# Kernel tuning notes

Measured on AMD Instinct MI355X. Metric: run time of the kernel, lower is better.

The kernel has to match this reference:

```python
import jax, jax.numpy as jnp
import numpy as np

B, L, D, H = 8, 1024, 1024, 16
DPH = D // H  # 64


def setup_inputs() -> dict:
    key = jax.random.key(0)
    ks = jax.random.split(key, 12)
    s = 1.0 / np.sqrt(D)
    return {
        "key": jax.random.normal(ks[0], (B, L, D), jnp.float32),
        "value": jax.random.normal(ks[1], (B, L, D), jnp.float32),
        "query": jax.random.normal(ks[2], (B, L, D), jnp.float32),
        "attn_mask": jax.random.randint(ks[3], (B, L, L), 0, 2) > 0,
        "Wq": jax.random.normal(ks[4], (D, D), jnp.float32) * s,
        "bq": jnp.zeros((D,), jnp.float32),
        "Wk": jax.random.normal(ks[5], (D, D), jnp.float32) * s,
        "bk": jnp.zeros((D,), jnp.float32),
        "Wv": jax.random.normal(ks[6], (D, D), jnp.float32) * s,
        "bv": jnp.zeros((D,), jnp.float32),
        "Wo": jax.random.normal(ks[7], (D, D), jnp.float32) * s,
        "bo": jnp.zeros((D,), jnp.float32),
        "gamma": jnp.ones((D,), jnp.float32),
        "beta": jnp.zeros((D,), jnp.float32),
    }


def _layer_norm(x, gamma, beta, eps=1e-5):
    mu = jnp.mean(x, axis=-1, keepdims=True)
    var = jnp.var(x, axis=-1, keepdims=True)
    return (x - mu) * jax.lax.rsqrt(var + eps) * gamma + beta


def reference(key, value, query, attn_mask, Wq, bq, Wk, bk, Wv, bv, Wo, bo, gamma, beta):
    residual = query
    k = key @ Wk + bk      # [B, L, D]
    v = value @ Wv + bv
    q = query @ Wq + bq
    # faithful to torch: raw row-major view into [B*H, L, dph] (NOT standard head transpose)
    k = k.reshape(B * H, -1, DPH)
    v = v.reshape(B * H, -1, DPH)
    q = q.reshape(B * H, -1, DPH)
    # faithful to torch repeat: tile whole batch H times along dim 0
    mask = jnp.tile(attn_mask, (H, 1, 1))  # [B*H, L, L]
    scale = DPH ** (-0.5)
    scores = jnp.einsum('bqd,bkd->bqk', q, k) * scale
    scores = jnp.where(mask, jnp.float32(-1e9), scores)
    attention = jax.nn.softmax(scores, axis=2)
    context = jnp.einsum('bqk,bkd->bqd', attention, v)  # [B*H, L, dph]
    context = context.reshape(B, -1, D)
    output = context @ Wo + bo
    output = _layer_norm(residual + output, gamma, beta)
    return (output, attention)
```

## Files before the change

### kernel.cpp

```cpp
#include <hip/hip_runtime.h>

typedef __attribute__((ext_vector_type(8))) short short8;
typedef __attribute__((ext_vector_type(4))) float f32x4;

#define AS1C(p) ((const __attribute__((address_space(1))) void*)(p))
#define AS3(p)  ((__attribute__((address_space(3))) void*)(p))

__device__ __forceinline__ unsigned short f2bf(float f) {
  unsigned int u = __float_as_uint(f);
  return (unsigned short)((u + 0x7fffu + ((u >> 16) & 1u)) >> 16);
}

__device__ __forceinline__ void gload16(const void* g, void* l) {
  __builtin_amdgcn_global_load_lds(AS1C(g), AS3(l), 16, 0, 0);
}

#define EXP_C 0.18033688011112042f

__global__ __launch_bounds__(256) void conv3_bf16(const float* __restrict__ s0,
                                                  const float* __restrict__ s1,
                                                  const float* __restrict__ s2,
                                                  unsigned short* __restrict__ d0,
                                                  unsigned short* __restrict__ d1,
                                                  unsigned short* __restrict__ d2, int n4) {
  const float* in = (blockIdx.z == 0) ? s0 : (blockIdx.z == 1) ? s1 : s2;
  unsigned short* out = (blockIdx.z == 0) ? d0 : (blockIdx.z == 1) ? d1 : d2;
  int i = blockIdx.x * 256 + threadIdx.x;
  if (i >= n4) return;
  float4 v = ((const float4*)in)[i];
  ushort4 o;
  o.x = f2bf(v.x); o.y = f2bf(v.y); o.z = f2bf(v.z); o.w = f2bf(v.w);
  ((ushort4*)out)[i] = o;
}

__global__ __launch_bounds__(256) void pack_mask_kernel(const int* __restrict__ m,
                                                        unsigned int* __restrict__ bits) {
  int i = blockIdx.x * 256 + threadIdx.x;
  unsigned long long bl = __ballot(m[i] != 0);
  if ((threadIdx.x & 63) == 0) {
    bits[(i >> 5)]     = (unsigned int)bl;
    bits[(i >> 5) + 1] = (unsigned int)(bl >> 32);
  }
}

__global__ __launch_bounds__(256) void transpose_w(const float* __restrict__ W0,
                                                   const float* __restrict__ W1,
                                                   const float* __restrict__ W2,
                                                   const float* __restrict__ W3,
                                                   unsigned short* __restrict__ WtBase) {
  __shared__ float t[32][33];
  const float* W = (blockIdx.z == 0) ? W0 : (blockIdx.z == 1) ? W1 : (blockIdx.z == 2) ? W2 : W3;
  unsigned short* Wt = WtBase + (size_t)blockIdx.z * 1024 * 1024;
  int bx = blockIdx.x * 32, by = blockIdx.y * 32;
  int tx = threadIdx.x & 31, ty = threadIdx.x >> 5;
#pragma unroll
  for (int i = 0; i < 4; ++i) {
    int r = ty + i * 8;
    t[r][tx] = W[(size_t)(by + r) * 1024 + bx + tx];
  }
  __syncthreads();
#pragma unroll
  for (int i = 0; i < 4; ++i) {
    int r = ty + i * 8;
    Wt[(size_t)(bx + r) * 1024 + by + tx] = f2bf(t[tx][r]);
  }
}

__global__ __launch_bounds__(256) void transpose_v(const unsigned short* __restrict__ v,
                                                   unsigned short* __restrict__ vt) {
  __shared__ unsigned short t[32][33];
  int b = blockIdx.z;
  int bx = blockIdx.x * 32;
  int by = blockIdx.y * 32;
  int tx = threadIdx.x & 31, ty = threadIdx.x >> 5;
#pragma unroll
  for (int i = 0; i < 4; ++i) {
    int r = ty + i * 8;
    t[r][tx] = v[(size_t)b * 65536 + (size_t)(by + r) * 64 + bx + tx];
  }
  __syncthreads();
#pragma unroll
  for (int i = 0; i < 4; ++i) {
    int r = ty + i * 8;
    vt[(size_t)b * 65536 + (size_t)(bx + r) * 1024 + by + tx] = t[tx][r];
  }
}

template <int MODE>
__device__ __forceinline__ void gemm_body(
    const unsigned short* __restrict__ A, const unsigned short* __restrict__ Bt,
    const float* __restrict__ bias, const float* __restrict__ res,
    unsigned short* __restrict__ Cb, float* __restrict__ Cf,
    unsigned short* lA, unsigned short* lB) {
  const int K = 1024, N = 1024;
  const int tid = threadIdx.x;
  const int wave = tid >> 6, lane = tid & 63;
  const int row_l = lane & 15, kg = lane >> 4;
  const int wg = blockIdx.y * 8 + blockIdx.x;
  const int idx = (wg & 7) * 64 + (wg >> 3);
  const int m0 = (idx >> 3) * 128, n0 = (idx & 7) * 128;
  const int wm = (wave >> 1) * 64, wn = (wave & 1) * 64;
  f32x4 acc[4][4] = {};

  for (int k0 = 0; k0 < K; k0 += 32) {
    __syncthreads();
#pragma unroll
    for (int it = 0; it < 2; ++it) {
      int c = wave * 64 + it * 256 + lane;
      int r = c >> 2, ch = c & 3;
      int sch = ch ^ (r & 3);
      gload16(A + (size_t)(m0 + r) * K + k0 + sch * 8, lA + (wave * 64 + it * 256) * 8);
      gload16(Bt + (size_t)(n0 + r) * K + k0 + sch * 8, lB + (wave * 64 + it * 256) * 8);
    }
    __syncthreads();
    short8 af[4], bfr[4];
#pragma unroll
    for (int t = 0; t < 4; ++t) {
      int ra = wm + t * 16 + row_l;
      af[t] = *(const short8*)(lA + ra * 32 + ((kg ^ (ra & 3)) << 3));
      int rb = wn + t * 16 + row_l;
      bfr[t] = *(const short8*)(lB + rb * 32 + ((kg ^ (rb & 3)) << 3));
    }
    __builtin_amdgcn_s_setprio(1);
#pragma unroll
    for (int mt = 0; mt < 4; ++mt)
#pragma unroll
      for (int nt = 0; nt < 4; ++nt)
        acc[mt][nt] = __builtin_amdgcn_mfma_f32_16x16x32_bf16(af[mt], bfr[nt], acc[mt][nt], 0, 0, 0);
    __builtin_amdgcn_s_setprio(0);
  }
#pragma unroll
  for (int mt = 0; mt < 4; ++mt)
#pragma unroll
    for (int nt = 0; nt < 4; ++nt)
#pragma unroll
      for (int r = 0; r < 4; ++r) {
        int grow = m0 + wm + mt * 16 + kg * 4 + r;
        int gcol = n0 + wn + nt * 16 + row_l;
        float v = acc[mt][nt][r] + bias[gcol];
        if (MODE == 0) {
          Cb[(size_t)grow * N + gcol] = f2bf(v);
        } else {
          v += res[(size_t)grow * N + gcol];
          Cf[(size_t)grow * N + gcol] = v;
        }
      }
}

__global__ __launch_bounds__(256) void gemm_qk_kernel(
    const unsigned short* __restrict__ A0, const unsigned short* __restrict__ A1,
    const unsigned short* __restrict__ WtBase,
    const float* __restrict__ b0, const float* __restrict__ b1,
    unsigned short* __restrict__ C0, unsigned short* __restrict__ C1) {
  __shared__ unsigned short lA[128 * 32];
  __shared__ unsigned short lB[128 * 32];
  int z = blockIdx.z;
  const unsigned short* A = (z == 0) ? A0 : A1;
  const float* bias = (z == 0) ? b0 : b1;
  unsigned short* C = (z == 0) ? C0 : C1;
  gemm_body<0>(A, WtBase + (size_t)z * 1024 * 1024, bias, nullptr, C, nullptr, lA, lB);
}

__global__ __launch_bounds__(256) void gemm_proj_kernel(
    const unsigned short* __restrict__ A, const unsigned short* __restrict__ Bt,
    const float* __restrict__ bias, unsigned short* __restrict__ Cb) {
  __shared__ unsigned short lA[128 * 32];
  __shared__ unsigned short lB[128 * 32];
  gemm_body<0>(A, Bt, bias, nullptr, Cb, nullptr, lA, lB);
}

__global__ __launch_bounds__(256) void gemm_out_kernel(
    const unsigned short* __restrict__ A, const unsigned short* __restrict__ Bt,
    const float* __restrict__ bias, const float* __restrict__ res, float* __restrict__ Cf) {
  __shared__ unsigned short lA[128 * 32];
  __shared__ unsigned short lB[128 * 32];
  gemm_body<1>(A, Bt, bias, res, nullptr, Cf, lA, lB);
}

__global__ __launch_bounds__(256) void attn_kernel(
    const unsigned short* __restrict__ Q,
    const unsigned short* __restrict__ Km,
    const unsigned short* __restrict__ Vt,
    const unsigned int* __restrict__ mbits,
    float* __restrict__ attn,
    unsigned short* __restrict__ ctx) {
  __shared__ unsigned short lQ[64 * 64];
  __shared__ unsigned short lK[64 * 64];
  __shared__ unsigned short lV[64 * 64];
  __shared__ unsigned short lP[64 * 64];
  const int tid = threadIdx.x, wave = tid >> 6, lane = tid & 63;
  const int row_l = lane & 15, kg = lane >> 4;
  const int wg = blockIdx.y * 16 + blockIdx.x;
  const int idx = (wg & 7) * 256 + (wg >> 3);
  const int batch = idx >> 4, qt = idx & 15;
  const int q0 = qt * 64;
  const unsigned short* Qb = Q + (size_t)batch * 65536;
  const unsigned short* Kb = Km + (size_t)batch * 65536;
  const unsigned short* Vb = Vt + (size_t)batch * 65536;
  const unsigned int* mrow = mbits + (size_t)(batch & 7) * 32768;
  float* attb = attn + (size_t)batch * 1048576;

#pragma unroll
  for (int it = 0; it < 2; ++it) {
    int c = wave * 64 + it * 256 + lane;
    int r = c >> 3, ch = c & 7;
    int sch = ch ^ (r & 7);
    gload16(Qb + (size_t)(q0 + r) * 64 + sch * 8, lQ + (wave * 64 + it * 256) * 8);
  }
  __syncthreads();
  short8 qf[2];
  {
    int rq = wave * 16 + row_l;
#pragma unroll
    for (int kk = 0; kk < 2; ++kk)
      qf[kk] = *(const short8*)(lQ + rq * 64 + (((kk * 4 + kg) ^ (rq & 7)) << 3));
  }

  float l_part[4] = {0.f, 0.f, 0.f, 0.f};
  const int qrow_base = q0 + wave * 16 + kg * 4;

  for (int kt = 0; kt < 16; ++kt) {
    __syncthreads();
#pragma unroll
    for (int it = 0; it < 2; ++it) {
      int c = wave * 64 + it * 256 + lane;
      int r = c >> 3, ch = c & 7;
      int sch = ch ^ (r & 7);
      gload16(Kb + (size_t)(kt * 64 + r) * 64 + sch * 8, lK + (wave * 64 + it * 256) * 8);
    }
    __syncthreads();
    f32x4 s[4];
    __builtin_amdgcn_s_setprio(1);
#pragma unroll
    for (int cf = 0; cf < 4; ++cf) {
      int rk = cf * 16 + row_l;
      f32x4 a = {0.f, 0.f, 0.f, 0.f};
#pragma unroll
      for (int kk = 0; kk < 2; ++kk) {
        short8 kf = *(const short8*)(lK + rk * 64 + (((kk * 4 + kg) ^ (rk & 7)) << 3));
        a = __builtin_amdgcn_mfma_f32_16x16x32_bf16(qf[kk], kf, a, 0, 0, 0);
      }
      s[cf] = a;
    }
    __builtin_amdgcn_s_setprio(0);
#pragma unroll
    for (int r = 0; r < 4; ++r) {
      unsigned int w0 = mrow[(qrow_base + r) * 32 + kt * 2];
      unsigned int w1 = mrow[(qrow_base + r) * 32 + kt * 2 + 1];
#pragma unroll
      for (int cf = 0; cf < 4; ++cf) {
        int kl = cf * 16 + row_l;
        unsigned int w = (kl & 32) ? w1 : w0;
        int bit = (w >> (kl & 31)) & 1;
        float e = __builtin_exp2f(s[cf][r] * EXP_C);
        l_part[r] += bit ? 0.f : e;
      }
    }
  }
  float il[4];
#pragma unroll
  for (int r = 0; r < 4; ++r) {
    float se = l_part[r];
#pragma unroll
    for (int sh = 1; sh < 16; sh <<= 1) se += __shfl_xor(se, sh);
    il[r] = 1.f / se;
  }

  f32x4 cacc[4] = {};

  for (int kt = 0; kt < 16; ++kt) {
    __syncthreads();
#pragma unroll
    for (int it = 0; it < 2; ++it) {
      int c = wave * 64 + it * 256 + lane;
      int r = c >> 3, ch = c & 7;
      int sch = ch ^ (r & 7);
      gload16(Kb + (size_t)(kt * 64 + r) * 64 + sch * 8, lK + (wave * 64 + it * 256) * 8);
      gload16(Vb + (size_t)r * 1024 + kt * 64 + sch * 8, lV + (wave * 64 + it * 256) * 8);
    }
    __syncthreads();
    f32x4 s[4];
    __builtin_amdgcn_s_setprio(1);
#pragma unroll
    for (int cf = 0; cf < 4; ++cf) {
      int rk = cf * 16 + row_l;
      f32x4 a = {0.f, 0.f, 0.f, 0.f};
#pragma unroll
      for (int kk = 0; kk < 2; ++kk) {
        short8 kf = *(const short8*)(lK + rk * 64 + (((kk * 4 + kg) ^ (rk & 7)) << 3));
        a = __builtin_amdgcn_mfma_f32_16x16x32_bf16(qf[kk], kf, a, 0, 0, 0);
      }
      s[cf] = a;
    }
    __builtin_amdgcn_s_setprio(0);
#pragma unroll
    for (int r = 0; r < 4; ++r) {
      unsigned int w0 = mrow[(qrow_base + r) * 32 + kt * 2];
      unsigned int w1 = mrow[(qrow_base + r) * 32 + kt * 2 + 1];
      float* arow = attb + (size_t)(qrow_base + r) * 1024 + kt * 64;
      int prow = wave * 16 + kg * 4 + r;
#pragma unroll
      for (int cf = 0; cf < 4; ++cf) {
        int kl = cf * 16 + row_l;
        unsigned int w = (kl & 32) ? w1 : w0;
        int bit = (w >> (kl & 31)) & 1;
        float e = __builtin_exp2f(s[cf][r] * EXP_C) * il[r];
        float p = bit ? 0.f : e;
        __builtin_nontemporal_store(p, arow + kl);
        int pch = (kl >> 3) ^ (prow & 7);
        lP[prow * 64 + pch * 8 + (kl & 7)] = f2bf(p);
      }
    }
    __syncthreads();
    __builtin_amdgcn_s_setprio(1);
#pragma unroll
    for (int kk = 0; kk < 2; ++kk) {
      int rp = wave * 16 + row_l;
      short8 pa = *(const short8*)(lP + rp * 64 + (((kk * 4 + kg) ^ (rp & 7)) << 3));
#pragma unroll
      for (int df = 0; df < 4; ++df) {
        int rv = df * 16 + row_l;
        short8 vb = *(const short8*)(lV + rv * 64 + (((kk * 4 + kg) ^ (rv & 7)) << 3));
        cacc[df] = __builtin_amdgcn_mfma_f32_16x16x32_bf16(pa, vb, cacc[df], 0, 0, 0);
      }
    }
    __builtin_amdgcn_s_setprio(0);
  }
#pragma unroll
  for (int df = 0; df < 4; ++df)
#pragma unroll
    for (int r = 0; r < 4; ++r) {
      int grow = q0 + wave * 16 + kg * 4 + r;
      int gcol = df * 16 + row_l;
      ctx[(size_t)batch * 65536 + (size_t)grow * 64 + gcol] = f2bf(cacc[df][r]);
    }
}

__global__ __launch_bounds__(256) void layernorm_kernel(float* __restrict__ io,
                                                        const float* __restrict__ gamma,
                                                        const float* __restrict__ beta) {
  int wave = threadIdx.x >> 6, lane = threadIdx.x & 63;
  size_t row = (size_t)blockIdx.x * 4 + wave;
  float* p = io + row * 1024;
  float4 v[4];
  float s = 0.f, ss = 0.f;
#pragma unroll
  for (int i = 0; i < 4; ++i) {
    v[i] = ((const float4*)p)[lane + i * 64];
    s += v[i].x + v[i].y + v[i].z + v[i].w;
    ss += v[i].x * v[i].x + v[i].y * v[i].y + v[i].z * v[i].z + v[i].w * v[i].w;
  }
#pragma unroll
  for (int m = 1; m < 64; m <<= 1) { s += __shfl_xor(s, m); ss += __shfl_xor(ss, m); }
  float mu = s * (1.f / 1024.f);
  float var = ss * (1.f / 1024.f) - mu * mu;
  float rinv = rsqrtf(var + 1e-5f);
#pragma unroll
  for (int i = 0; i < 4; ++i) {
    int idx = lane + i * 64;
    float4 g = ((const float4*)gamma)[idx];
    float4 b = ((const float4*)beta)[idx];
    float4 o;
    o.x = (v[i].x - mu) * rinv * g.x + b.x;
    o.y = (v[i].y - mu) * rinv * g.y + b.y;
    o.z = (v[i].z - mu) * rinv * g.z + b.z;
    o.w = (v[i].w - mu) * rinv * g.w + b.w;
    ((float4*)p)[idx] = o;
  }
}

extern "C" void kernel_launch(void* const* d_in, const int* in_sizes, int n_in,
                              void* d_out, int out_size, void* d_ws, size_t ws_size,
                              hipStream_t stream) {
  const float* key   = (const float*)d_in[0];
  const float* value = (const float*)d_in[1];
  const float* query = (const float*)d_in[2];
  const int* amask   = (const int*)d_in[3];
  const float* Wq = (const float*)d_in[4];
  const float* bq = (const float*)d_in[5];
  const float* Wk = (const float*)d_in[6];
  const float* bk = (const float*)d_in[7];
  const float* Wv = (const float*)d_in[8];
  const float* bv = (const float*)d_in[9];
  const float* Wo = (const float*)d_in[10];
  const float* bo = (const float*)d_in[11];
  const float* gamma = (const float*)d_in[12];
  const float* beta  = (const float*)d_in[13];

  char* ws = (char*)d_ws;
  const size_t MB = 1024 * 1024;
  float* out_f = (float*)d_out;
  float* attn_f = (float*)d_out + (size_t)8388608;
  const int n4 = 8388608 / 4;
  dim3 gemm_grid(8, 64);
  dim3 gemm_grid2(8, 64, 2);
  dim3 attn_grid(16, 128);

  const bool big_ws = ws_size >= 106 * MB;
  if (big_ws) {
    unsigned short* A0 = (unsigned short*)(ws + 0);
    unsigned short* A1 = (unsigned short*)(ws + 16 * MB);
    unsigned short* A2 = (unsigned short*)(ws + 32 * MB);
    unsigned short* B1 = (unsigned short*)(ws + 48 * MB);
    unsigned short* B2 = (unsigned short*)(ws + 64 * MB);
    unsigned short* B3 = (unsigned short*)(ws + 80 * MB);
    unsigned short* Wts = (unsigned short*)(ws + 96 * MB);
    unsigned int* mbits = (unsigned int*)(ws + 104 * MB);

    transpose_w<<<dim3(32, 32, 4), 256, 0, stream>>>(Wq, Wk, Wv, Wo, Wts);
    pack_mask_kernel<<<32768, 256, 0, stream>>>(amask, mbits);
    conv3_bf16<<<dim3(8192, 1, 3), 256, 0, stream>>>(query, key, value, A0, A1, A2, n4);
    gemm_qk_kernel<<<gemm_grid2, 256, 0, stream>>>(A0, A1, Wts, bq, bk, B1, B2);
    gemm_proj_kernel<<<gemm_grid, 256, 0, stream>>>(A2, Wts + 2 * MB, bv, B3);
    transpose_v<<<dim3(2, 32, 128), 256, 0, stream>>>(B3, A1);
    attn_kernel<<<attn_grid, 256, 0, stream>>>(B1, B2, A1, mbits, attn_f, A2);
    gemm_out_kernel<<<gemm_grid, 256, 0, stream>>>(A2, Wts + 3 * MB, bo, query, out_f);
    layernorm_kernel<<<2048, 256, 0, stream>>>(out_f, gamma, beta);
  } else {
    unsigned short* B0 = (unsigned short*)(ws + 0);
    unsigned short* B1 = (unsigned short*)(ws + 16 * MB);
    unsigned short* B2 = (unsigned short*)(ws + 32 * MB);
    unsigned short* B3 = (unsigned short*)(ws + 48 * MB);
    unsigned short* Wts = (unsigned short*)(ws + 64 * MB);
    unsigned int* mbits = (unsigned int*)(ws + 72 * MB);

    transpose_w<<<dim3(32, 32, 4), 256, 0, stream>>>(Wq, Wk, Wv, Wo, Wts);
    pack_mask_kernel<<<32768, 256, 0, stream>>>(amask, mbits);
    conv3_bf16<<<dim3(8192, 1, 1), 256, 0, stream>>>(query, query, query, B0, B0, B0, n4);
    gemm_qk_kernel<<<gemm_grid, 256, 0, stream>>>(B0, B0, Wts, bq, bq, B1, B1);
    conv3_bf16<<<dim3(8192, 1, 1), 256, 0, stream>>>(key, key, key, B0, B0, B0, n4);
    gemm_qk_kernel<<<gemm_grid, 256, 0, stream>>>(B0, B0, Wts + 1 * MB, bk, bk, B2, B2);
    conv3_bf16<<<dim3(8192, 1, 1), 256, 0, stream>>>(value, value, value, B0, B0, B0, n4);
    gemm_proj_kernel<<<gemm_grid, 256, 0, stream>>>(B0, Wts + 2 * MB, bv, B3);
    transpose_v<<<dim3(2, 32, 128), 256, 0, stream>>>(B3, B0);
    attn_kernel<<<attn_grid, 256, 0, stream>>>(B1, B2, B0, mbits, attn_f, B3);
    gemm_out_kernel<<<gemm_grid, 256, 0, stream>>>(B3, Wts + 3 * MB, bo, query, out_f);
    layernorm_kernel<<<2048, 256, 0, stream>>>(out_f, gamma, beta);
  }
}
```

Measured before the change: 364.0 us.

## Double-buffer K tiles in attention pass one and drop redundant barriers

The attention kernel's first pass (softmax denominator) now double-buffers K tiles, using the V LDS buffer as the second stage, so the global-to-LDS load of the next tile overlaps the MFMA and exp work on the current one. The separate P buffer is removed and the Q LDS buffer is reused for P, since Q fragments already sit in registers. The barrier between writing P and the PV MFMAs is dropped because each wave only reads its own rows of P. __syncthreads waits are replaced by an explicit vmcnt(0) wait plus s_barrier. These cut load stalls and barrier count, and the smaller LDS footprint may allow more resident blocks. The cost is more dependence on careful wave-local ordering to stay correct.

```diff
diff --git a/kernel.cpp b/kernel.cpp
--- a/kernel.cpp
+++ b/kernel.cpp
@@ -187,7 +187,6 @@
   __shared__ unsigned short lQ[64 * 64];
   __shared__ unsigned short lK[64 * 64];
   __shared__ unsigned short lV[64 * 64];
-  __shared__ unsigned short lP[64 * 64];
   const int tid = threadIdx.x, wave = tid >> 6, lane = tid & 63;
   const int row_l = lane & 15, kg = lane >> 4;
   const int wg = blockIdx.y * 16 + blockIdx.x;
@@ -199,6 +198,29 @@
   const unsigned short* Vb = Vt + (size_t)batch * 65536;
   const unsigned int* mrow = mbits + (size_t)(batch & 7) * 32768;
   float* attb = attn + (size_t)batch * 1048576;
+  const int qrow_base = q0 + wave * 16 + kg * 4;
+
+#define STAGE_K_TO(kt, dst)                                                           \
+  {                                                                                   \
+    _Pragma("unroll") for (int it = 0; it < 2; ++it) {                                \
+      int c = wave * 64 + it * 256 + lane;                                            \
+      int r_ = c >> 3, ch_ = c & 7, sch_ = ch_ ^ (r_ & 7);                            \
+      gload16(Kb + (size_t)((kt) * 64 + r_) * 64 + sch_ * 8,                          \
+              (dst) + (wave * 64 + it * 256) * 8);                                    \
+    }                                                                                 \
+  }
+#define STAGE_V_TO(kt, dst)                                                           \
+  {                                                                                   \
+    _Pragma("unroll") for (int it = 0; it < 2; ++it) {                                \
+      int c = wave * 64 + it * 256 + lane;                                            \
+      int r_ = c >> 3, ch_ = c & 7, sch_ = ch_ ^ (r_ & 7);                            \
+      gload16(Vb + (size_t)r_ * 1024 + (kt) * 64 + sch_ * 8,                          \
+              (dst) + (wave * 64 + it * 256) * 8);                                    \
+    }                                                                                 \
+  }
+#define WAIT_BAR0                                             \
+  asm volatile("s_waitcnt vmcnt(0)" ::: "memory");            \
+  __builtin_amdgcn_s_barrier();
 
 #pragma unroll
   for (int it = 0; it < 2; ++it) {
@@ -207,7 +229,8 @@
     int sch = ch ^ (r & 7);
     gload16(Qb + (size_t)(q0 + r) * 64 + sch * 8, lQ + (wave * 64 + it * 256) * 8);
   }
-  __syncthreads();
+  STAGE_K_TO(0, lK)
+  WAIT_BAR0
   short8 qf[2];
   {
     int rq = wave * 16 + row_l;
@@ -217,18 +240,8 @@
   }
 
   float l_part[4] = {0.f, 0.f, 0.f, 0.f};
-  const int qrow_base = q0 + wave * 16 + kg * 4;
-
-  for (int kt = 0; kt < 16; ++kt) {
-    __syncthreads();
-#pragma unroll
-    for (int it = 0; it < 2; ++it) {
-      int c = wave * 64 + it * 256 + lane;
-      int r = c >> 3, ch = c & 7;
-      int sch = ch ^ (r & 7);
-      gload16(Kb + (size_t)(kt * 64 + r) * 64 + sch * 8, lK + (wave * 64 + it * 256) * 8);
-    }
-    __syncthreads();
+
+  auto pass1_step = [&](const unsigned short* kbuf, int kt) {
     f32x4 s[4];
     __builtin_amdgcn_s_setprio(1);
 #pragma unroll
@@ -237,7 +250,7 @@
       f32x4 a = {0.f, 0.f, 0.f, 0.f};
 #pragma unroll
       for (int kk = 0; kk < 2; ++kk) {
-        short8 kf = *(const short8*)(lK + rk * 64 + (((kk * 4 + kg) ^ (rk & 7)) << 3));
+        short8 kf = *(const short8*)(kbuf + rk * 64 + (((kk * 4 + kg) ^ (rk & 7)) << 3));
         a = __builtin_amdgcn_mfma_f32_16x16x32_bf16(qf[kk], kf, a, 0, 0, 0);
       }
       s[cf] = a;
@@ -256,6 +269,14 @@
         l_part[r] += bit ? 0.f : e;
       }
     }
+  };
+  for (int kt2 = 0; kt2 < 16; kt2 += 2) {
+    STAGE_K_TO(kt2 + 1, lV)
+    pass1_step(lK, kt2);
+    WAIT_BAR0
+    if (kt2 + 2 < 16) STAGE_K_TO(kt2 + 2, lK)
+    pass1_step(lV, kt2 + 1);
+    WAIT_BAR0
   }
   float il[4];
 #pragma unroll
@@ -267,18 +288,13 @@
   }
 
   f32x4 cacc[4] = {};
+  unsigned short* lP = lQ;
 
   for (int kt = 0; kt < 16; ++kt) {
     __syncthreads();
-#pragma unroll
-    for (int it = 0; it < 2; ++it) {
-      int c = wave * 64 + it * 256 + lane;
-      int r = c >> 3, ch = c & 7;
-      int sch = ch ^ (r & 7);
-      gload16(Kb + (size_t)(kt * 64 + r) * 64 + sch * 8, lK + (wave * 64 + it * 256) * 8);
-      gload16(Vb + (size_t)r * 1024 + kt * 64 + sch * 8, lV + (wave * 64 + it * 256) * 8);
-    }
-    __syncthreads();
+    STAGE_K_TO(kt, lK)
+    STAGE_V_TO(kt, lV)
+    WAIT_BAR0
     f32x4 s[4];
     __builtin_amdgcn_s_setprio(1);
 #pragma unroll
@@ -311,7 +327,6 @@
         lP[prow * 64 + pch * 8 + (kl & 7)] = f2bf(p);
       }
     }
-    __syncthreads();
     __builtin_amdgcn_s_setprio(1);
 #pragma unroll
     for (int kk = 0; kk < 2; ++kk) {
@@ -334,6 +349,9 @@
       int gcol = df * 16 + row_l;
       ctx[(size_t)batch * 65536 + (size_t)grow * 64 + gcol] = f2bf(cacc[df][r]);
     }
+#undef STAGE_K_TO
+#undef STAGE_V_TO
+#undef WAIT_BAR0
 }
 
 __global__ __launch_bounds__(256) void layernorm_kernel(float* __restrict__ io,
```

Result: no change. 359.9 us (-1.1%).
